# Kernel tuning notes

Hardware: AMD Instinct MI355X
Metric: run time of the kernel (lower is better)

Reference implementation:

```python
import jax, jax.numpy as jnp
import numpy as np

HEADS = 16
TOPK = 2048  # dsa_topk


def setup_inputs() -> dict:
    key = jax.random.key(0)
    ks = jax.random.split(key, 9)
    B, Q, KV, C = 2, 2048, 16384, 1024
    w = lambda k: jax.random.normal(k, (C, C), dtype=jnp.float32) * 0.02
    return {
        "hidden_states": jax.random.normal(ks[0], (B, Q, C), dtype=jnp.float32),
        "encoder_hidden_states": jax.random.normal(ks[1], (B, KV, C), dtype=jnp.float32),
        "Wq": w(ks[2]),
        "Wk": w(ks[3]),
        "Wv": w(ks[4]),
        "Wo": w(ks[5]),
        "bo": jnp.zeros((C,), dtype=jnp.float32),
        "Wg": jax.random.normal(ks[6], (C, C), dtype=jnp.float32) * 0.01,  # xavier gain 0.1
        "bg": jnp.full((C,), -1.5, dtype=jnp.float32),  # gate_init_bias
    }


def reference(hidden_states, encoder_hidden_states, Wq, Wk, Wv, Wo, bo, Wg, bg):
    B, Q, C = hidden_states.shape
    H = HEADS
    D = C // H
    scale = 1.0 / jnp.sqrt(jnp.asarray(D, dtype=hidden_states.dtype))

    # projections -> [B, H, S, D]
    q = (hidden_states @ Wq).reshape(B, Q, H, D).transpose(0, 2, 1, 3)
    k = (encoder_hidden_states @ Wk).reshape(B, -1, H, D).transpose(0, 2, 1, 3)
    v = (encoder_hidden_states @ Wv).reshape(B, -1, H, D).transpose(0, 2, 1, 3)

    # _sparse_select: query-summary scored top-k KV gather (kv_len > TOPK here)
    q_summary = q.mean(axis=2)                                   # [B, H, D]
    sel_score = jnp.einsum("bhd,bhkd->bhk", q_summary, k) * scale
    idx = jax.lax.top_k(sel_score, TOPK)[1]                      # [B, H, TOPK]
    k_sel = jnp.take_along_axis(k, idx[..., None], axis=2)       # [B, H, TOPK, D]
    v_sel = jnp.take_along_axis(v, idx[..., None], axis=2)

    # attention over selected KV
    scores = jnp.einsum("bhqd,bhkd->bhqk", q, k_sel) * scale
    probs = jax.nn.softmax(scores.astype(jnp.float32), axis=-1).astype(scores.dtype)
    out = jnp.einsum("bhqk,bhkd->bhqd", probs, v_sel)
    out = out.transpose(0, 2, 1, 3).reshape(B, Q, C)

    # sigmoid gate + output projection (to_out[1] dropout is identity at eval)
    out = out * jax.nn.sigmoid(out @ Wg + bg)
    out = out @ Wo + bo

    # residual_connection=True, rescale_output_factor=1.0
    return out + hidden_states
```

## Files before the change

kernel.cpp:

```cpp
#include <hip/hip_runtime.h>
#include <hip/hip_bf16.h>

typedef unsigned short u16;
typedef __bf16 bf16x8 __attribute__((ext_vector_type(8)));
typedef float f32x4 __attribute__((ext_vector_type(4)));

__device__ __forceinline__ u16 f2bf(float f) {
    union { float f; unsigned int u; } v; v.f = f;
    unsigned int u = v.u;
    unsigned int r = (u + 0x7fffu + ((u >> 16) & 1u)) >> 16;
    return (u16)r;
}
__device__ __forceinline__ float bf2f(u16 b) {
    union { unsigned int u; float f; } v; v.u = ((unsigned int)b) << 16;
    return v.f;
}

__device__ __forceinline__ void glds16(const u16* g, u16* l) {
    __builtin_amdgcn_global_load_lds(
        (__attribute__((address_space(1))) void*)(g),
        (__attribute__((address_space(3))) void*)(l), 16, 0, 0);
}

__global__ __launch_bounds__(256) void cast_bf16_kernel(const float* __restrict__ src,
                                                        u16* __restrict__ dst, int n4) {
    int i = blockIdx.x * 256 + threadIdx.x;
    if (i >= n4) return;
    float4 v = ((const float4*)src)[i];
    ushort4 o;
    o.x = f2bf(v.x); o.y = f2bf(v.y); o.z = f2bf(v.z); o.w = f2bf(v.w);
    ((ushort4*)dst)[i] = o;
}

__global__ __launch_bounds__(256) void transpose_cast_kernel(
    const float* __restrict__ Wq, const float* __restrict__ Wk, const float* __restrict__ Wv,
    const float* __restrict__ Wg, const float* __restrict__ Wo,
    u16* __restrict__ WqT, u16* __restrict__ WkvT, u16* __restrict__ WgT, u16* __restrict__ WoT) {
    __shared__ float tile[32][33];
    const float* src; u16* dst;
    switch (blockIdx.z) {
        case 0: src = Wq; dst = WqT; break;
        case 1: src = Wk; dst = WkvT; break;
        case 2: src = Wv; dst = WkvT + (size_t)1024 * 1024; break;
        case 3: src = Wg; dst = WgT; break;
        default: src = Wo; dst = WoT; break;
    }
    int n0 = blockIdx.x * 32, k0 = blockIdx.y * 32;
    int tx = threadIdx.x, ty = threadIdx.y;
    #pragma unroll
    for (int j = 0; j < 4; j++)
        tile[ty + j * 8][tx] = src[(size_t)(k0 + ty + j * 8) * 1024 + n0 + tx];
    __syncthreads();
    #pragma unroll
    for (int j = 0; j < 4; j++)
        dst[(size_t)(n0 + ty + j * 8) * 1024 + k0 + tx] = f2bf(tile[tx][ty + j * 8]);
}

template <int EPI>
__global__ __launch_bounds__(256) void gemm_bf16(
    const u16* __restrict__ A, const u16* __restrict__ B, int ldc,
    u16* __restrict__ Cbf, const float* __restrict__ bias,
    const u16* __restrict__ mul_src, const float* __restrict__ add_src,
    float* __restrict__ Cf) {
    constexpr int K = 1024;
    const int tid = threadIdx.x;
    const int w = tid >> 6, l = tid & 63;
    const int lr = l & 15, lg = l >> 4;
    const int wr = w >> 1, wc = w & 1;
    const int m0 = blockIdx.y * 128, n0 = blockIdx.x * 128;

    __shared__ u16 As[128 * 64];
    __shared__ u16 Bs[128 * 64];

    const f32x4 fz = {0.f, 0.f, 0.f, 0.f};
    f32x4 acc[4][4];
    #pragma unroll
    for (int i = 0; i < 4; i++)
        #pragma unroll
        for (int j = 0; j < 4; j++) acc[i][j] = fz;

    const int lane_row = l >> 3;
    const int lane_sl  = l & 7;
    const int src_ch   = lane_sl ^ lane_row;
    const u16* Ab = A + (size_t)(m0 + w * 32 + lane_row) * K + src_ch * 8;
    const u16* Bb = B + (size_t)(n0 + w * 32 + lane_row) * K + src_ch * 8;

    for (int kt = 0; kt < K; kt += 64) {
        __syncthreads();
        #pragma unroll
        for (int j = 0; j < 4; j++) {
            glds16(Ab + (size_t)j * 8 * K + kt, As + (w * 32 + j * 8) * 64);
            glds16(Bb + (size_t)j * 8 * K + kt, Bs + (w * 32 + j * 8) * 64);
        }
        __syncthreads();
        #pragma unroll
        for (int kk = 0; kk < 2; kk++) {
            bf16x8 af[4], bfr[4];
            #pragma unroll
            for (int mi = 0; mi < 4; mi++) {
                int row = wr * 64 + mi * 16 + lr;
                int ch = (kk * 4 + lg) ^ (row & 7);
                af[mi] = *(const bf16x8*)(As + row * 64 + ch * 8);
            }
            #pragma unroll
            for (int ni = 0; ni < 4; ni++) {
                int row = wc * 64 + ni * 16 + lr;
                int ch = (kk * 4 + lg) ^ (row & 7);
                bfr[ni] = *(const bf16x8*)(Bs + row * 64 + ch * 8);
            }
            #pragma unroll
            for (int mi = 0; mi < 4; mi++)
                #pragma unroll
                for (int ni = 0; ni < 4; ni++)
                    acc[mi][ni] = __builtin_amdgcn_mfma_f32_16x16x32_bf16(
                        af[mi], bfr[ni], acc[mi][ni], 0, 0, 0);
        }
    }

    #pragma unroll
    for (int mi = 0; mi < 4; mi++) {
        #pragma unroll
        for (int ni = 0; ni < 4; ni++) {
            #pragma unroll
            for (int r = 0; r < 4; r++) {
                int gm = m0 + wr * 64 + mi * 16 + lg * 4 + r;
                int gn = n0 + wc * 64 + ni * 16 + lr;
                float v = acc[mi][ni][r];
                if (EPI == 0) {
                    Cbf[(size_t)gm * ldc + gn] = f2bf(v);
                } else if (EPI == 2) {
                    float g = v + bias[gn];
                    float a = bf2f(mul_src[(size_t)gm * ldc + gn]);
                    float sg = 1.f / (1.f + __expf(-g));
                    Cbf[(size_t)gm * ldc + gn] = f2bf(a * sg);
                } else {
                    Cf[(size_t)gm * ldc + gn] = v + bias[gn] + add_src[(size_t)gm * ldc + gn];
                }
            }
        }
    }
}

__global__ __launch_bounds__(256) void hsum1_kernel(const float* __restrict__ hidden,
                                                    float* __restrict__ part) {
    int b = blockIdx.x, chunk = blockIdx.y;
    int tid = threadIdx.x;
    const float4* src = (const float4*)(hidden + ((size_t)b * 2048 + chunk * 16) * 1024) + tid;
    float4 acc = {0.f, 0.f, 0.f, 0.f};
    #pragma unroll
    for (int r = 0; r < 16; r++) {
        float4 v = src[r * 256];
        acc.x += v.x; acc.y += v.y; acc.z += v.z; acc.w += v.w;
    }
    ((float4*)(part + ((size_t)b * 128 + chunk) * 1024))[tid] = acc;
}

__global__ __launch_bounds__(256) void hsum2_kernel(const float* __restrict__ part,
                                                    float* __restrict__ hm) {
    int b = blockIdx.x, tid = threadIdx.x;
    const float4* src = (const float4*)(part + (size_t)b * 128 * 1024) + tid;
    float4 acc = {0.f, 0.f, 0.f, 0.f};
    for (int c = 0; c < 128; c++) {
        float4 v = src[c * 256];
        acc.x += v.x; acc.y += v.y; acc.z += v.z; acc.w += v.w;
    }
    const float inv = 1.f / 2048.f;
    acc.x *= inv; acc.y *= inv; acc.z *= inv; acc.w *= inv;
    ((float4*)(hm + (size_t)b * 1024))[tid] = acc;
}

__global__ __launch_bounds__(256) void qz_kernel(const float* __restrict__ hm,
                                                 const u16* __restrict__ WqT,
                                                 const u16* __restrict__ WkT,
                                                 u16* __restrict__ z_bf) {
    int bh = blockIdx.x, b = bh >> 4, h = bh & 15;
    int tid = threadIdx.x;
    __shared__ float hm_l[1024];
    __shared__ float qs_l[64];
    __shared__ float red[256];
    ((float4*)hm_l)[tid] = ((const float4*)(hm + (size_t)b * 1024))[tid];
    __syncthreads();
    {
        int d = tid >> 2, q = tid & 3;
        const u16* wq = WqT + (size_t)(h * 64 + d) * 1024 + q * 256;
        float a = 0.f;
        for (int i = 0; i < 256; i += 8) {
            uint4 u = *(const uint4*)(wq + i);
            const u16* p = (const u16*)&u;
            #pragma unroll
            for (int j = 0; j < 8; j++) a += bf2f(p[j]) * hm_l[q * 256 + i + j];
        }
        red[tid] = a;
    }
    __syncthreads();
    if (tid < 64)
        qs_l[tid] = red[tid * 4] + red[tid * 4 + 1] + red[tid * 4 + 2] + red[tid * 4 + 3];
    __syncthreads();
    {
        float z0 = 0.f, z1 = 0.f, z2 = 0.f, z3 = 0.f;
        for (int d = 0; d < 64; d++) {
            float qs = qs_l[d];
            const u16* wk = WkT + (size_t)(h * 64 + d) * 1024 + tid * 4;
            uint2 u = *(const uint2*)wk;
            const u16* p = (const u16*)&u;
            z0 += qs * bf2f(p[0]); z1 += qs * bf2f(p[1]);
            z2 += qs * bf2f(p[2]); z3 += qs * bf2f(p[3]);
        }
        ushort4 o;
        o.x = f2bf(z0); o.y = f2bf(z1); o.z = f2bf(z2); o.w = f2bf(z3);
        *(ushort4*)(z_bf + (size_t)bh * 1024 + tid * 4) = o;
    }
}

__global__ __launch_bounds__(256) void score_kernel(const u16* __restrict__ ebf,
                                                    const u16* __restrict__ z_bf,
                                                    float* __restrict__ score) {
    const int b = blockIdx.y, kv0 = blockIdx.x * 64;
    const int tid = threadIdx.x, w = tid >> 6, l = tid & 63;
    const int lr = l & 15, lg = l >> 4;
    __shared__ u16 e_lds[2][64 * 64];

    const u16* eb = ebf + (size_t)(b * 16384 + kv0) * 1024;
    const u16* zb = z_bf + (size_t)b * 16 * 1024;
    const int lrow = l >> 3, lch = l & 7;
    const int src_ch = lch ^ lrow;

    auto stage = [&](int kt, int buf) {
        const u16* s0 = eb + (size_t)(w * 16 + lrow) * 1024 + kt + src_ch * 8;
        glds16(s0,            e_lds[buf] + (w * 16) * 64);
        glds16(s0 + 8 * 1024, e_lds[buf] + (w * 16 + 8) * 64);
    };
    stage(0, 0);

    const f32x4 fz = {0.f, 0.f, 0.f, 0.f};
    f32x4 acc = fz;

    #pragma unroll 1
    for (int t = 0; t < 16; ++t) {
        const int kt = t * 64;
        if (t + 1 < 16) {
            stage(kt + 64, (t & 1) ^ 1);
            asm volatile("s_waitcnt vmcnt(2)" ::: "memory");
        } else {
            asm volatile("s_waitcnt vmcnt(0)" ::: "memory");
        }
        __builtin_amdgcn_sched_barrier(0);
        const u16* ecur = e_lds[t & 1];
        #pragma unroll
        for (int ks = 0; ks < 2; ks++) {
            bf16x8 af = *(const bf16x8*)(zb + (size_t)lr * 1024 + kt + ks * 32 + lg * 8);
            int row = w * 16 + lr;
            bf16x8 bf_ = *(const bf16x8*)(ecur + row * 64 + (((ks * 4 + lg) ^ (row & 7))) * 8);
            acc = __builtin_amdgcn_mfma_f32_16x16x32_bf16(af, bf_, acc, 0, 0, 0);
        }
    }
    #pragma unroll
    for (int r = 0; r < 4; r++)
        score[(size_t)(b * 16 + lg * 4 + r) * 16384 + kv0 + w * 16 + lr] = acc[r];
}

__global__ __launch_bounds__(1024) void select_kernel(const float* __restrict__ score,
                                                      int* __restrict__ sel_idx) {
    const int bh = blockIdx.x;
    const float* sc = score + (size_t)bh * 16384;
    const int tid = threadIdx.x;
    const int grp = tid >> 8;

    __shared__ int hist[4][256];
    __shared__ int total[256];
    __shared__ int bc[4];

    u16 key[16];
    #pragma unroll
    for (int j = 0; j < 16; j++) {
        unsigned int b = __float_as_uint(sc[tid + j * 1024]);
        unsigned int ui = (b & 0x80000000u) ? ~b : (b | 0x80000000u);
        key[j] = (u16)(ui >> 16);
    }

    ((int*)hist)[tid] = 0;
    __syncthreads();
    #pragma unroll
    for (int j = 0; j < 16; j++) atomicAdd(&hist[grp][key[j] >> 8], 1);
    __syncthreads();
    if (tid < 256) total[tid] = hist[0][tid] + hist[1][tid] + hist[2][tid] + hist[3][tid];
    __syncthreads();
    if (tid == 0) {
        int want = 2048, acc = 0;
        for (int dd = 255; dd >= 0; dd--) {
            acc += total[dd];
            if (acc >= want) { bc[0] = dd; bc[1] = want - (acc - total[dd]); break; }
        }
    }
    __syncthreads();
    const int hi = bc[0];
    const int want1 = bc[1];

    ((int*)hist)[tid] = 0;
    __syncthreads();
    #pragma unroll
    for (int j = 0; j < 16; j++)
        if ((key[j] >> 8) == hi) atomicAdd(&hist[grp][key[j] & 0xff], 1);
    __syncthreads();
    if (tid < 256) total[tid] = hist[0][tid] + hist[1][tid] + hist[2][tid] + hist[3][tid];
    __syncthreads();
    if (tid == 0) {
        int want = want1, acc = 0;
        for (int dd = 255; dd >= 0; dd--) {
            acc += total[dd];
            if (acc >= want) { bc[0] = (hi << 8) | dd; bc[1] = want - (acc - total[dd]); break; }
        }
        bc[2] = 0; bc[3] = 0;
    }
    __syncthreads();
    const u16 thr = (u16)bc[0];
    const int n_eq = bc[1];
    const int base_eq = 2048 - n_eq;

    int* out = sel_idx + (size_t)bh * 2048;
    #pragma unroll
    for (int j = 0; j < 16; j++) {
        int i = tid + j * 1024;
        if (key[j] > thr) {
            int p = atomicAdd(&bc[2], 1);
            out[p] = i;
        } else if (key[j] == thr) {
            int p = atomicAdd(&bc[3], 1);
            if (p < n_eq) out[base_eq + p] = i;
        }
    }
}

__global__ __launch_bounds__(256) void selproj_kernel(const u16* __restrict__ ebf,
                                                      const u16* __restrict__ WkvT,
                                                      const int* __restrict__ sel_idx,
                                                      u16* __restrict__ k_sel,
                                                      u16* __restrict__ v_selT) {
    const int bh = blockIdx.y, b = bh >> 4, h = bh & 15;
    const int t0 = blockIdx.x * 128;
    const int tid = threadIdx.x, w = tid >> 6, l = tid & 63;
    const int lr = l & 15, lg = l >> 4;
    const int lane_row = l >> 3, src_ch = (l & 7) ^ lane_row;

    __shared__ u16 e_lds[2][128 * 64];
    __shared__ u16 w_lds[2][128 * 64];

    int encrow[4], wrow[4];
    #pragma unroll
    for (int j = 0; j < 4; j++) {
        int t = t0 + w * 32 + j * 8 + lane_row;
        encrow[j] = b * 16384 + sel_idx[(size_t)bh * 2048 + t];
        int r = w * 32 + j * 8 + lane_row;
        wrow[j] = (r < 64) ? (h * 64 + r) : (1024 + h * 64 + (r & 63));
    }

    auto stage = [&](int kt, int buf) {
        #pragma unroll
        for (int j = 0; j < 4; j++) {
            glds16(ebf + (size_t)encrow[j] * 1024 + kt + src_ch * 8,
                   e_lds[buf] + (w * 32 + j * 8) * 64);
            glds16(WkvT + (size_t)wrow[j] * 1024 + kt + src_ch * 8,
                   w_lds[buf] + (w * 32 + j * 8) * 64);
        }
    };

    const f32x4 fz = {0.f, 0.f, 0.f, 0.f};
    f32x4 acc_k[2][4], acc_v[8];
    #pragma unroll
    for (int i = 0; i < 2; i++)
        #pragma unroll
        for (int j = 0; j < 4; j++) acc_k[i][j] = fz;
    #pragma unroll
    for (int i = 0; i < 8; i++) acc_v[i] = fz;

    stage(0, 0);
    __syncthreads();

    #pragma unroll 1
    for (int t = 0; t < 16; ++t) {
        const int kt = t * 64;
        const int cur = t & 1;
        if (t + 1 < 16) stage(kt + 64, cur ^ 1);

        const u16* ec = e_lds[cur];
        const u16* wc_ = w_lds[cur];
        __builtin_amdgcn_s_setprio(1);
        #pragma unroll
        for (int ks = 0; ks < 2; ks++) {
            bf16x8 ae[2];
            #pragma unroll
            for (int mi = 0; mi < 2; mi++) {
                int row = w * 32 + mi * 16 + lr;
                ae[mi] = *(const bf16x8*)(ec + row * 64 + (((ks * 4 + lg) ^ (row & 7))) * 8);
            }
            bf16x8 aw;
            {
                int row = 64 + w * 16 + lr;
                aw = *(const bf16x8*)(wc_ + row * 64 + (((ks * 4 + lg) ^ (row & 7))) * 8);
            }
            #pragma unroll
            for (int ni = 0; ni < 4; ni++) {
                int row = ni * 16 + lr;
                bf16x8 bw = *(const bf16x8*)(wc_ + row * 64 + (((ks * 4 + lg) ^ (row & 7))) * 8);
                acc_k[0][ni] = __builtin_amdgcn_mfma_f32_16x16x32_bf16(ae[0], bw, acc_k[0][ni], 0, 0, 0);
                acc_k[1][ni] = __builtin_amdgcn_mfma_f32_16x16x32_bf16(ae[1], bw, acc_k[1][ni], 0, 0, 0);
            }
            #pragma unroll
            for (int ni = 0; ni < 8; ni++) {
                int row = ni * 16 + lr;
                bf16x8 be = *(const bf16x8*)(ec + row * 64 + (((ks * 4 + lg) ^ (row & 7))) * 8);
                acc_v[ni] = __builtin_amdgcn_mfma_f32_16x16x32_bf16(aw, be, acc_v[ni], 0, 0, 0);
            }
        }
        __builtin_amdgcn_s_setprio(0);
        __syncthreads();
    }

    u16* kb = k_sel + (size_t)bh * 2048 * 64;
    #pragma unroll
    for (int mi = 0; mi < 2; mi++)
        #pragma unroll
        for (int ni = 0; ni < 4; ni++)
            #pragma unroll
            for (int r = 0; r < 4; r++) {
                int t = t0 + w * 32 + mi * 16 + lg * 4 + r;
                int d = ni * 16 + lr;
                kb[(size_t)t * 64 + (((d >> 3) ^ (t & 7)) * 8) + (d & 7)] = f2bf(acc_k[mi][ni][r]);
            }
    u16* vb = v_selT + (size_t)bh * 64 * 2048;
    #pragma unroll
    for (int ni = 0; ni < 8; ni++)
        #pragma unroll
        for (int r = 0; r < 4; r++) {
            int d = w * 16 + lg * 4 + r;
            int t = t0 + ni * 16 + lr;
            int tl = t & 63;
            int kap = (tl & 15) * 4 + (tl >> 4);
            vb[(size_t)d * 2048 + (t & ~63) + (((kap >> 3) ^ (d & 7)) * 8) + (kap & 7)] =
                f2bf(acc_v[ni][r]);
        }
}

__global__ __launch_bounds__(512) void attn_kernel(
    const u16* __restrict__ q_bf, const u16* __restrict__ k_sel,
    const u16* __restrict__ v_selT, u16* __restrict__ attn_out) {
    const int bh = blockIdx.y, b = bh >> 4, h = bh & 15;
    const int q0 = blockIdx.x * 128;
    const int tid = threadIdx.x, w = tid >> 6, l = tid & 63;
    const int lr = l & 15, lg = l >> 4;
    const int lk = lr & 7;
    const float SC = 0.18033688011f;
    const float THR = 11.0f;

    __shared__ u16 k_lds[2][64 * 64];
    __shared__ u16 vt_lds[64 * 64];
    __shared__ u16 p_lds[8][16][68];

    const u16* qb = q_bf + ((size_t)b * 2048 + q0 + w * 16 + lr) * 1024 + h * 64;
    bf16x8 qf0 = *(const bf16x8*)(qb + lg * 8);
    bf16x8 qf1 = *(const bf16x8*)(qb + 32 + lg * 8);

    const f32x4 fz = {0.f, 0.f, 0.f, 0.f};
    f32x4 o[4];
    #pragma unroll
    for (int f = 0; f < 4; f++) o[f] = fz;
    float mm = -1e30f;
    float l_part[4] = {0.f, 0.f, 0.f, 0.f};

    const u16* kb  = k_sel + (size_t)bh * 2048 * 64;
    const u16* vtb = v_selT + (size_t)bh * 64 * 2048;

    auto stageK = [&](int it, int buf) {
        const u16* ksrc = kb + (size_t)(it * 64 + w * 8) * 64 + (size_t)l * 8;
        glds16(ksrc, k_lds[buf] + (w * 8) * 64);
    };
    auto stageV = [&](int it) {
        const u16* vsrc = vtb + (size_t)(w * 8 + (l >> 3)) * 2048 + it * 64 + (l & 7) * 8;
        glds16(vsrc, vt_lds + (w * 8) * 64);
    };

    stageK(0, 0);
    __syncthreads();

    #pragma unroll 1
    for (int it = 0; it < 32; ++it) {
        const int cur = it & 1;
        stageV(it);
        if (it + 1 < 32) stageK(it + 1, cur ^ 1);

        f32x4 s[4];
        #pragma unroll
        for (int c = 0; c < 4; c++) s[c] = fz;
        __builtin_amdgcn_s_setprio(1);
        #pragma unroll
        for (int c = 0; c < 4; c++) {
            const u16* krow = k_lds[cur] + (c * 16 + lr) * 64;
            bf16x8 kf0 = *(const bf16x8*)(krow + (lg ^ lk) * 8);
            s[c] = __builtin_amdgcn_mfma_f32_16x16x32_bf16(qf0, kf0, s[c], 0, 0, 0);
            bf16x8 kf1 = *(const bf16x8*)(krow + (((4 + lg) ^ lk)) * 8);
            s[c] = __builtin_amdgcn_mfma_f32_16x16x32_bf16(qf1, kf1, s[c], 0, 0, 0);
        }
        __builtin_amdgcn_s_setprio(0);

        float mx = s[0][0];
        #pragma unroll
        for (int c = 0; c < 4; c++)
            #pragma unroll
            for (int r = 0; r < 4; r++) mx = fmaxf(mx, s[c][r]);
        mx = fmaxf(mx, __shfl_xor(mx, 1));
        mx = fmaxf(mx, __shfl_xor(mx, 2));
        mx = fmaxf(mx, __shfl_xor(mx, 4));
        mx = fmaxf(mx, __shfl_xor(mx, 8));
        mx = fmaxf(mx, __shfl_xor(mx, 16));
        mx = fmaxf(mx, __shfl_xor(mx, 32));
        mx *= SC;
        if (mx > mm + THR) {
            float al = __builtin_amdgcn_exp2f(mm - mx);
            mm = mx;
            #pragma unroll
            for (int r = 0; r < 4; r++) l_part[r] *= al;
            #pragma unroll
            for (int f = 0; f < 4; f++)
                #pragma unroll
                for (int r = 0; r < 4; r++) o[f][r] *= al;
        }
        #pragma unroll
        for (int r = 0; r < 4; r++) {
            ushort4 pk;
            u16 pb[4];
            #pragma unroll
            for (int c = 0; c < 4; c++) {
                float p = __builtin_amdgcn_exp2f(__builtin_fmaf(s[c][r], SC, -mm));
                l_part[r] += p;
                __bf16 hv = (__bf16)p;
                pb[c] = *(u16*)&hv;
            }
            pk.x = pb[0]; pk.y = pb[1]; pk.z = pb[2]; pk.w = pb[3];
            *(ushort4*)(&p_lds[w][lg * 4 + r][lr * 4]) = pk;
        }

        if (it + 1 < 32) {
            asm volatile("s_waitcnt vmcnt(1)" ::: "memory");
        } else {
            asm volatile("s_waitcnt vmcnt(0)" ::: "memory");
        }
        __builtin_amdgcn_sched_barrier(0);
        __builtin_amdgcn_s_barrier();

        __builtin_amdgcn_s_setprio(1);
        #pragma unroll
        for (int kk = 0; kk < 2; kk++) {
            bf16x8 ap = *(const bf16x8*)(&p_lds[w][lr][kk * 32 + lg * 8]);
            #pragma unroll
            for (int f = 0; f < 4; f++) {
                const u16* vrow = vt_lds + (f * 16 + lr) * 64;
                bf16x8 bv = *(const bf16x8*)(vrow + (((kk * 4 + lg) ^ lk)) * 8);
                o[f] = __builtin_amdgcn_mfma_f32_16x16x32_bf16(ap, bv, o[f], 0, 0, 0);
            }
        }
        __builtin_amdgcn_s_setprio(0);

        __syncthreads();
    }

    float invl[4];
    #pragma unroll
    for (int r = 0; r < 4; r++) {
        float lr_ = l_part[r];
        lr_ += __shfl_xor(lr_, 1);
        lr_ += __shfl_xor(lr_, 2);
        lr_ += __shfl_xor(lr_, 4);
        lr_ += __shfl_xor(lr_, 8);
        invl[r] = 1.f / lr_;
    }
    u16* ob = attn_out + ((size_t)b * 2048 + q0 + w * 16 + lg * 4) * 1024 + h * 64 + lr;
    #pragma unroll
    for (int f = 0; f < 4; f++) {
        #pragma unroll
        for (int r = 0; r < 4; r++) {
            __bf16 hv = (__bf16)(o[f][r] * invl[r]);
            ob[(size_t)r * 1024 + f * 16] = *(u16*)&hv;
        }
    }
}

extern "C" void kernel_launch(void* const* d_in, const int* in_sizes, int n_in,
                              void* d_out, int out_size, void* d_ws, size_t ws_size,
                              hipStream_t stream) {
    const float* hidden = (const float*)d_in[0];
    const float* enc    = (const float*)d_in[1];
    const float* Wq = (const float*)d_in[2];
    const float* Wk = (const float*)d_in[3];
    const float* Wv = (const float*)d_in[4];
    const float* Wo = (const float*)d_in[5];
    const float* bo = (const float*)d_in[6];
    const float* Wg = (const float*)d_in[7];
    const float* bg = (const float*)d_in[8];
    float* out = (float*)d_out;

    char* ws = (char*)d_ws;
    size_t off = 0;
    auto alloc = [&](size_t bytes) -> char* {
        char* p = ws + off;
        off += (bytes + 255) & ~(size_t)255;
        return p;
    };
    u16* hbf   = (u16*)alloc(4096ull * 1024 * 2);
    u16* ebf   = (u16*)alloc(32768ull * 1024 * 2);
    u16* WqT   = (u16*)alloc(1024ull * 1024 * 2);
    u16* WkvT  = (u16*)alloc(2048ull * 1024 * 2);
    u16* WgT   = (u16*)alloc(1024ull * 1024 * 2);
    u16* WoT   = (u16*)alloc(1024ull * 1024 * 2);
    u16* q_bf  = (u16*)alloc(4096ull * 1024 * 2);
    float* hm  = (float*)alloc(2ull * 1024 * 4);
    float* part = (float*)alloc(2ull * 128 * 1024 * 4);
    u16* z_bf  = (u16*)alloc(32ull * 1024 * 2);
    float* scor = (float*)alloc(32ull * 16384 * 4);
    int* sel    = (int*)alloc(32ull * 2048 * 4);
    u16* ksel   = (u16*)alloc(32ull * 2048 * 64 * 2);
    u16* vT     = (u16*)alloc(32ull * 64 * 2048 * 2);
    u16* attn   = (u16*)alloc(4096ull * 1024 * 2);
    u16* gate   = (u16*)alloc(4096ull * 1024 * 2);
    (void)ws_size; (void)in_sizes; (void)n_in; (void)out_size;

    hsum1_kernel<<<dim3(2, 128), 256, 0, stream>>>(hidden, part);
    hsum2_kernel<<<2, 256, 0, stream>>>(part, hm);
    cast_bf16_kernel<<<4096, 256, 0, stream>>>(hidden, hbf, 1048576);
    cast_bf16_kernel<<<32768, 256, 0, stream>>>(enc, ebf, 8388608);
    transpose_cast_kernel<<<dim3(32, 32, 5), dim3(32, 8), 0, stream>>>(
        Wq, Wk, Wv, Wg, Wo, WqT, WkvT, WgT, WoT);

    qz_kernel<<<32, 256, 0, stream>>>(hm, WqT, WkvT, z_bf);
    score_kernel<<<dim3(256, 2), 256, 0, stream>>>(ebf, z_bf, scor);
    select_kernel<<<32, 1024, 0, stream>>>(scor, sel);
    selproj_kernel<<<dim3(16, 32), 256, 0, stream>>>(ebf, WkvT, sel, ksel, vT);

    gemm_bf16<0><<<dim3(8, 32), 256, 0, stream>>>(hbf, WqT, 1024, q_bf, nullptr, nullptr, nullptr, nullptr);
    attn_kernel<<<dim3(16, 32), 512, 0, stream>>>(q_bf, ksel, vT, attn);

    gemm_bf16<2><<<dim3(8, 32), 256, 0, stream>>>(attn, WgT, 1024, gate, bg, attn, nullptr, nullptr);
    gemm_bf16<3><<<dim3(8, 32), 256, 0, stream>>>(gate, WoT, 1024, nullptr, bo, nullptr, hidden, out);
}
```

Before: 253.0 us.

## Fuse hidden cast with column sum, fold mean into qz, single-buffer selproj

Merges the hidden-state bf16 cast and partial column sum into one prep kernel, which saves a read of the hidden states and a launch. The second reduction stage moves into qz_kernel, where each of 32 blocks now re-reduces the 128 partials redundantly. selproj_kernel drops its double-buffered LDS staging and the setprio hints in favour of a single buffer with two barriers per step. That removes the load/compute overlap in the gather projection, which may hurt it, but halves its LDS use.

```diff
diff --git a/kernel.cpp b/kernel.cpp
--- a/kernel.cpp
+++ b/kernel.cpp
@@ -30,6 +30,25 @@
     ushort4 o;
     o.x = f2bf(v.x); o.y = f2bf(v.y); o.z = f2bf(v.z); o.w = f2bf(v.w);
     ((ushort4*)dst)[i] = o;
+}
+
+__global__ __launch_bounds__(256) void prep_kernel(const float* __restrict__ hidden,
+                                                   u16* __restrict__ hbf,
+                                                   float* __restrict__ part) {
+    int b = blockIdx.x, chunk = blockIdx.y;
+    int tid = threadIdx.x;
+    const float4* src = (const float4*)(hidden + ((size_t)b * 2048 + chunk * 16) * 1024) + tid;
+    u16* dst = hbf + ((size_t)b * 2048 + chunk * 16) * 1024 + tid * 4;
+    float4 acc = {0.f, 0.f, 0.f, 0.f};
+    #pragma unroll
+    for (int r = 0; r < 16; r++) {
+        float4 v = src[r * 256];
+        acc.x += v.x; acc.y += v.y; acc.z += v.z; acc.w += v.w;
+        ushort4 o;
+        o.x = f2bf(v.x); o.y = f2bf(v.y); o.z = f2bf(v.z); o.w = f2bf(v.w);
+        *(ushort4*)(dst + (size_t)r * 1024) = o;
+    }
+    ((float4*)(part + ((size_t)b * 128 + chunk) * 1024))[tid] = acc;
 }
 
 __global__ __launch_bounds__(256) void transpose_cast_kernel(
@@ -141,35 +160,7 @@
     }
 }
 
-__global__ __launch_bounds__(256) void hsum1_kernel(const float* __restrict__ hidden,
-                                                    float* __restrict__ part) {
-    int b = blockIdx.x, chunk = blockIdx.y;
-    int tid = threadIdx.x;
-    const float4* src = (const float4*)(hidden + ((size_t)b * 2048 + chunk * 16) * 1024) + tid;
-    float4 acc = {0.f, 0.f, 0.f, 0.f};
-    #pragma unroll
-    for (int r = 0; r < 16; r++) {
-        float4 v = src[r * 256];
-        acc.x += v.x; acc.y += v.y; acc.z += v.z; acc.w += v.w;
-    }
-    ((float4*)(part + ((size_t)b * 128 + chunk) * 1024))[tid] = acc;
-}
-
-__global__ __launch_bounds__(256) void hsum2_kernel(const float* __restrict__ part,
-                                                    float* __restrict__ hm) {
-    int b = blockIdx.x, tid = threadIdx.x;
-    const float4* src = (const float4*)(part + (size_t)b * 128 * 1024) + tid;
-    float4 acc = {0.f, 0.f, 0.f, 0.f};
-    for (int c = 0; c < 128; c++) {
-        float4 v = src[c * 256];
-        acc.x += v.x; acc.y += v.y; acc.z += v.z; acc.w += v.w;
-    }
-    const float inv = 1.f / 2048.f;
-    acc.x *= inv; acc.y *= inv; acc.z *= inv; acc.w *= inv;
-    ((float4*)(hm + (size_t)b * 1024))[tid] = acc;
-}
-
-__global__ __launch_bounds__(256) void qz_kernel(const float* __restrict__ hm,
+__global__ __launch_bounds__(256) void qz_kernel(const float* __restrict__ part,
                                                  const u16* __restrict__ WqT,
                                                  const u16* __restrict__ WkT,
                                                  u16* __restrict__ z_bf) {
@@ -178,7 +169,17 @@
     __shared__ float hm_l[1024];
     __shared__ float qs_l[64];
     __shared__ float red[256];
-    ((float4*)hm_l)[tid] = ((const float4*)(hm + (size_t)b * 1024))[tid];
+    {
+        const float4* src = (const float4*)(part + (size_t)b * 128 * 1024) + tid;
+        float4 acc = {0.f, 0.f, 0.f, 0.f};
+        for (int c = 0; c < 128; c++) {
+            float4 v = src[c * 256];
+            acc.x += v.x; acc.y += v.y; acc.z += v.z; acc.w += v.w;
+        }
+        const float inv = 1.f / 2048.f;
+        acc.x *= inv; acc.y *= inv; acc.z *= inv; acc.w *= inv;
+        ((float4*)hm_l)[tid] = acc;
+    }
     __syncthreads();
     {
         int d = tid >> 2, q = tid & 3;
@@ -342,8 +343,8 @@
     const int lr = l & 15, lg = l >> 4;
     const int lane_row = l >> 3, src_ch = (l & 7) ^ lane_row;
 
-    __shared__ u16 e_lds[2][128 * 64];
-    __shared__ u16 w_lds[2][128 * 64];
+    __shared__ u16 e_lds[128 * 64];
+    __shared__ u16 w_lds[128 * 64];
 
     int encrow[4], wrow[4];
     #pragma unroll
@@ -354,16 +355,6 @@
         wrow[j] = (r < 64) ? (h * 64 + r) : (1024 + h * 64 + (r & 63));
     }
 
-    auto stage = [&](int kt, int buf) {
-        #pragma unroll
-        for (int j = 0; j < 4; j++) {
-            glds16(ebf + (size_t)encrow[j] * 1024 + kt + src_ch * 8,
-                   e_lds[buf] + (w * 32 + j * 8) * 64);
-            glds16(WkvT + (size_t)wrow[j] * 1024 + kt + src_ch * 8,
-                   w_lds[buf] + (w * 32 + j * 8) * 64);
-        }
-    };
-
     const f32x4 fz = {0.f, 0.f, 0.f, 0.f};
     f32x4 acc_k[2][4], acc_v[8];
     #pragma unroll
@@ -373,47 +364,41 @@
     #pragma unroll
     for (int i = 0; i < 8; i++) acc_v[i] = fz;
 
-    stage(0, 0);
-    __syncthreads();
-
-    #pragma unroll 1
-    for (int t = 0; t < 16; ++t) {
-        const int kt = t * 64;
-        const int cur = t & 1;
-        if (t + 1 < 16) stage(kt + 64, cur ^ 1);
-
-        const u16* ec = e_lds[cur];
-        const u16* wc_ = w_lds[cur];
-        __builtin_amdgcn_s_setprio(1);
+    for (int kt = 0; kt < 1024; kt += 64) {
+        __syncthreads();
+        #pragma unroll
+        for (int j = 0; j < 4; j++) {
+            glds16(ebf + (size_t)encrow[j] * 1024 + kt + src_ch * 8, e_lds + (w * 32 + j * 8) * 64);
+            glds16(WkvT + (size_t)wrow[j] * 1024 + kt + src_ch * 8, w_lds + (w * 32 + j * 8) * 64);
+        }
+        __syncthreads();
         #pragma unroll
         for (int ks = 0; ks < 2; ks++) {
             bf16x8 ae[2];
             #pragma unroll
             for (int mi = 0; mi < 2; mi++) {
                 int row = w * 32 + mi * 16 + lr;
-                ae[mi] = *(const bf16x8*)(ec + row * 64 + (((ks * 4 + lg) ^ (row & 7))) * 8);
+                ae[mi] = *(const bf16x8*)(e_lds + row * 64 + (((ks * 4 + lg) ^ (row & 7))) * 8);
             }
             bf16x8 aw;
             {
                 int row = 64 + w * 16 + lr;
-                aw = *(const bf16x8*)(wc_ + row * 64 + (((ks * 4 + lg) ^ (row & 7))) * 8);
+                aw = *(const bf16x8*)(w_lds + row * 64 + (((ks * 4 + lg) ^ (row & 7))) * 8);
             }
             #pragma unroll
             for (int ni = 0; ni < 4; ni++) {
                 int row = ni * 16 + lr;
-                bf16x8 bw = *(const bf16x8*)(wc_ + row * 64 + (((ks * 4 + lg) ^ (row & 7))) * 8);
+                bf16x8 bw = *(const bf16x8*)(w_lds + row * 64 + (((ks * 4 + lg) ^ (row & 7))) * 8);
                 acc_k[0][ni] = __builtin_amdgcn_mfma_f32_16x16x32_bf16(ae[0], bw, acc_k[0][ni], 0, 0, 0);
                 acc_k[1][ni] = __builtin_amdgcn_mfma_f32_16x16x32_bf16(ae[1], bw, acc_k[1][ni], 0, 0, 0);
             }
             #pragma unroll
             for (int ni = 0; ni < 8; ni++) {
                 int row = ni * 16 + lr;
-                bf16x8 be = *(const bf16x8*)(ec + row * 64 + (((ks * 4 + lg) ^ (row & 7))) * 8);
+                bf16x8 be = *(const bf16x8*)(e_lds + row * 64 + (((ks * 4 + lg) ^ (row & 7))) * 8);
                 acc_v[ni] = __builtin_amdgcn_mfma_f32_16x16x32_bf16(aw, be, acc_v[ni], 0, 0, 0);
             }
         }
-        __builtin_amdgcn_s_setprio(0);
-        __syncthreads();
     }
 
     u16* kb = k_sel + (size_t)bh * 2048 * 64;
@@ -612,7 +597,6 @@
     u16* WgT   = (u16*)alloc(1024ull * 1024 * 2);
     u16* WoT   = (u16*)alloc(1024ull * 1024 * 2);
     u16* q_bf  = (u16*)alloc(4096ull * 1024 * 2);
-    float* hm  = (float*)alloc(2ull * 1024 * 4);
     float* part = (float*)alloc(2ull * 128 * 1024 * 4);
     u16* z_bf  = (u16*)alloc(32ull * 1024 * 2);
     float* scor = (float*)alloc(32ull * 16384 * 4);
@@ -623,14 +607,12 @@
     u16* gate   = (u16*)alloc(4096ull * 1024 * 2);
     (void)ws_size; (void)in_sizes; (void)n_in; (void)out_size;
 
-    hsum1_kernel<<<dim3(2, 128), 256, 0, stream>>>(hidden, part);
-    hsum2_kernel<<<2, 256, 0, stream>>>(part, hm);
-    cast_bf16_kernel<<<4096, 256, 0, stream>>>(hidden, hbf, 1048576);
+    prep_kernel<<<dim3(2, 128), 256, 0, stream>>>(hidden, hbf, part);
     cast_bf16_kernel<<<32768, 256, 0, stream>>>(enc, ebf, 8388608);
     transpose_cast_kernel<<<dim3(32, 32, 5), dim3(32, 8), 0, stream>>>(
         Wq, Wk, Wv, Wg, Wo, WqT, WkvT, WgT, WoT);
 
-    qz_kernel<<<32, 256, 0, stream>>>(hm, WqT, WkvT, z_bf);
+    qz_kernel<<<32, 256, 0, stream>>>(part, WqT, WkvT, z_bf);
     score_kernel<<<dim3(256, 2), 256, 0, stream>>>(ebf, z_bf, scor);
     select_kernel<<<32, 1024, 0, stream>>>(scor, sel);
     selproj_kernel<<<dim3(16, 32), 256, 0, stream>>>(ebf, WkvT, sel, ksel, vT);
```

New measurement: 249.5 us. Within noise of the previous version (-1.4%).
